# Performance work log

Measured on AMD Instinct MI355X. Metric: run time of the kernel, lower is better.

## Reference

```python
import jax, jax.numpy as jnp
import numpy as np

K = 3          # number of nearest neighbors (pointops.interpolation uses k=3)
CHUNK = 4096   # fine-point chunk size for blocked kNN (bounds peak memory)
EPS = 1e-8     # inverse-distance epsilon, matches pointops interpolation


def _interpolate(xyz1, xyz2, feature2):
    """3-NN inverse-distance weighted interpolation from coarse (xyz2, feature2)
    onto fine points xyz1. Single batch (offsets cover all points)."""
    n1 = xyz1.shape[0]
    x2_sq = jnp.sum(xyz2 * xyz2, axis=-1)  # [N2]
    chunks = xyz1.reshape(n1 // CHUNK, CHUNK, 3)

    def body(q):  # q: [CHUNK, 3]
        q_sq = jnp.sum(q * q, axis=-1, keepdims=True)          # [CHUNK, 1]
        d2 = q_sq + x2_sq[None, :] - 2.0 * (q @ xyz2.T)        # [CHUNK, N2]
        neg_d2, idx = jax.lax.top_k(-d2, K)                    # 3 smallest
        dist = jnp.sqrt(jnp.maximum(-neg_d2, 1e-12))           # euclidean
        w = 1.0 / (dist + EPS)
        w = w / jnp.sum(w, axis=-1, keepdims=True)             # [CHUNK, K]
        return jnp.einsum('qk,qkc->qc', w, feature2[idx])      # [CHUNK, C]

    out = jax.lax.map(body, chunks)  # [n_chunks, CHUNK, C]
    return out.reshape(n1, -1)


def setup_inputs() -> dict:
    key = jax.random.key(0)
    k1, k2, k3, k4, k5, k6 = jax.random.split(key, 6)
    N1, N2, C, OUT = 32768, 8192, 256, 256
    xyz1 = jax.random.normal(k1, (N1, 3), dtype=jnp.float32)
    xyz2 = jax.random.normal(k2, (N2, 3), dtype=jnp.float32)
    feature1 = jax.random.normal(k3, (N1, C), dtype=jnp.float32)
    feature2 = jax.random.normal(k4, (N2, C), dtype=jnp.float32)
    offset1 = jnp.array([N1], dtype=jnp.int32)
    offset2 = jnp.array([N2], dtype=jnp.int32)
    W = jax.random.normal(k5, (OUT, C), dtype=jnp.float32) * (1.0 / np.sqrt(C))
    b = jax.random.normal(k6, (OUT,), dtype=jnp.float32) * 0.01
    return {"xyz1": xyz1, "xyz2": xyz2, "feature1": feature1,
            "feature2": feature2, "offset1": offset1, "offset2": offset2,
            "W": W, "b": b}


def reference(xyz1, xyz2, feature1, feature2, offset1, offset2, W, b):
    interp = _interpolate(xyz1, xyz2, feature2)  # [N1, C]
    return interp @ W.T + b                      # nn.Linear(in_coarse, out)
```

## Files before the change

kernel.cpp:

```cpp
#include <hip/hip_runtime.h>


#define FLT_BIG 3.402823466e+38f
#define CAP     16
#define MARGIN  3e-5f

__device__ __forceinline__ float rlf(float v, int l) {
    return __uint_as_float((unsigned)__builtin_amdgcn_readlane((int)__float_as_uint(v), l));
}

__global__ __launch_bounds__(256) void prep_kernel(const float* __restrict__ xyz2,
                                                   float4* __restrict__ pack, int N2) {
    int j = blockIdx.x * 256 + threadIdx.x;
    if (j < N2) {
        float x = xyz2[3 * j + 0];
        float y = xyz2[3 * j + 1];
        float z = xyz2[3 * j + 2];
        float4 p;
        p.x = x; p.y = y; p.z = z;
        p.w = 0.5f * (x * x + y * y + z * z);
        pack[j] = p;
    }
}

__global__ __launch_bounds__(256) void gemm_nt_f32(const float* __restrict__ A,
                                                   const float* __restrict__ B,
                                                   float* __restrict__ C,
                                                   int M, int N, int K) {
    __shared__ float As[64][68];
    __shared__ float Bs[64][68];

    const int t  = threadIdx.x;
    const int tx = t & 15;
    const int ty = t >> 4;
    const int bm = blockIdx.x * 64;
    const int bn = blockIdx.y * 64;

    float acc[4][4] = {{0.f}};

    for (int kt = 0; kt < K; kt += 64) {
#pragma unroll
        for (int rr = 0; rr < 4; ++rr) {
            int r = ty + 16 * rr;
            int c = tx * 4;
            float4 av = *(const float4*)(A + (size_t)(bm + r) * K + kt + c);
            As[c + 0][r] = av.x;
            As[c + 1][r] = av.y;
            As[c + 2][r] = av.z;
            As[c + 3][r] = av.w;
            float4 bv = *(const float4*)(B + (size_t)(bn + r) * K + kt + c);
            Bs[c + 0][r] = bv.x;
            Bs[c + 1][r] = bv.y;
            Bs[c + 2][r] = bv.z;
            Bs[c + 3][r] = bv.w;
        }
        __syncthreads();

#pragma unroll 8
        for (int k = 0; k < 64; ++k) {
            float4 a4 = *(const float4*)&As[k][ty * 4];
            float4 b4 = *(const float4*)&Bs[k][tx * 4];
            float a[4] = {a4.x, a4.y, a4.z, a4.w};
            float b[4] = {b4.x, b4.y, b4.z, b4.w};
#pragma unroll
            for (int i = 0; i < 4; ++i)
#pragma unroll
                for (int j = 0; j < 4; ++j)
                    acc[i][j] = fmaf(a[i], b[j], acc[i][j]);
        }
        __syncthreads();
    }

#pragma unroll
    for (int i = 0; i < 4; ++i) {
        float4 v;
        v.x = acc[i][0]; v.y = acc[i][1]; v.z = acc[i][2]; v.w = acc[i][3];
        *(float4*)(C + (size_t)(bm + ty * 4 + i) * N + bn + tx * 4) = v;
    }
}

#define TOP4V_INSERT(mv)                                           \
    do {                                                           \
        float _x  = (mv);                                          \
        float _n0 = fminf(b0, _x);  float _y0 = fmaxf(b0, _x); b0 = _n0; \
        float _n1 = fminf(b1, _y0); float _y1 = fmaxf(b1, _y0); b1 = _n1; \
        float _n2 = fminf(b2, _y1); float _y2 = fmaxf(b2, _y1); b2 = _n2; \
        b3 = fminf(b3, _y2);                                       \
    } while (0)

#define TOP3JD_INSERT(dd, j)                                       \
    do {                                                           \
        bool lt2 = ((dd) < d2v) || ((dd) == d2v && (j) < j2);      \
        if (lt2) {                                                 \
            bool lt1 = ((dd) < d1) || ((dd) == d1 && (j) < j1);    \
            if (lt1) {                                             \
                d2v = d1; j2 = j1;                                 \
                bool lt0 = ((dd) < d0) || ((dd) == d0 && (j) < j0);\
                if (lt0) { d1 = d0; j1 = j0; d0 = (dd); j0 = (j); }\
                else     { d1 = (dd); j1 = (j); }                  \
            } else { d2v = (dd); j2 = (j); }                       \
        }                                                          \
    } while (0)

#define DECLS(s) float px##s, py##s, pz##s, pw##s;
#define LOADS(s) { float4 _p = pack[base + ((s) << 6) + lane]; \
                   px##s = _p.x; py##s = _p.y; pz##s = _p.z; pw##s = _p.w; }
#define SAMPW(s) samp[wave][((s) << 6) + lane] = make_float4(px##s, py##s, pz##s, pw##s);
#define SLOTF(s)                                                               \
    {                                                                          \
        float acc = fmaf(qxx, px##s, fmaf(qyy, py##s, fmaf(qzz, pz##s, tq))); \
        unsigned long long mk = __ballot(acc >= pw##s);                        \
        while (mk) {                                                           \
            int l = __builtin_ctzll(mk);                                       \
            mk &= mk - 1;                                                      \
            if (lane == 0 && cnt < CAP)                                        \
                ring[wave][q][cnt] = (unsigned short)(base + ((s) << 6) + l);  \
            ++cnt;                                                             \
        }                                                                      \
    }
#define X16(M) M(0) M(1) M(2) M(3) M(4) M(5) M(6) M(7) \
               M(8) M(9) M(10) M(11) M(12) M(13) M(14) M(15)
#define X4(M)  M(0) M(1) M(2) M(3)

__global__ __launch_bounds__(512) void knn_gather(const float* __restrict__ xyz1,
                                                  const float4* __restrict__ pack,
                                                  const float4* __restrict__ G4,
                                                  const float4* __restrict__ bias4,
                                                  float4* __restrict__ out4,
                                                  int N2) {
    __shared__ float4         samp[8][256];
    __shared__ float          md[8][64][4];
    __shared__ int            mi[8][64][3];
    __shared__ float          thr[64];
    __shared__ unsigned short ring[8][64][CAP];
    __shared__ unsigned short cnts[8][64];
    __shared__ float          swgt[64][3];
    __shared__ int            sidx[64][3];

    const int tid  = threadIdx.x;
    const int wave = __builtin_amdgcn_readfirstlane(tid >> 6);
    const int lane = tid & 63;
    const int fine = blockIdx.x * 64 + lane;

    const float qx = xyz1[3 * fine + 0];
    const float qy = xyz1[3 * fine + 1];
    const float qz = xyz1[3 * fine + 2];

    const int chunk = N2 >> 3;
    const int base  = wave * chunk;

    X16(DECLS)
    X16(LOADS)

    X4(SAMPW)
    __syncthreads();

    {
        float b0 = FLT_BIG, b1 = FLT_BIG, b2 = FLT_BIG, b3 = FLT_BIG;
        const float4* sp = samp[wave];
#pragma unroll 1
        for (int k = 0; k < 256; k += 4) {
            float4 p0 = sp[k + 0];
            float4 p1 = sp[k + 1];
            float4 p2 = sp[k + 2];
            float4 p3 = sp[k + 3];
            float m0 = p0.w - fmaf(qx, p0.x, fmaf(qy, p0.y, qz * p0.z));
            float m1 = p1.w - fmaf(qx, p1.x, fmaf(qy, p1.y, qz * p1.z));
            float m2 = p2.w - fmaf(qx, p2.x, fmaf(qy, p2.y, qz * p2.z));
            float m3 = p3.w - fmaf(qx, p3.x, fmaf(qy, p3.y, qz * p3.z));
            float mm = fminf(fminf(m0, m1), fminf(m2, m3));
            TOP4V_INSERT(mm);
        }
        md[wave][lane][0] = b0;
        md[wave][lane][1] = b1;
        md[wave][lane][2] = b2;
        md[wave][lane][3] = b3;
    }
    __syncthreads();

    if (tid < 64) {
        float b0 = FLT_BIG, b1 = FLT_BIG, b2 = FLT_BIG, b3 = FLT_BIG;
#pragma unroll
        for (int w = 0; w < 8; ++w)
#pragma unroll
            for (int k = 0; k < 4; ++k)
                TOP4V_INSERT(md[w][tid][k]);
        thr[tid] = b3 + MARGIN;
    }
    __syncthreads();

    {
        const float qt_own = thr[lane];
#pragma unroll 1
        for (int q = 0; q < 64; ++q) {
            float qxx = rlf(qx, q);
            float qyy = rlf(qy, q);
            float qzz = rlf(qz, q);
            float tq  = rlf(qt_own, q);
            int cnt = 0;
            X16(SLOTF)
            if (lane == 0) cnts[wave][q] = (unsigned short)(cnt < CAP ? cnt : CAP);
        }
    }
    __syncthreads();

    {
        const int q  = tid >> 3;
        const int w  = tid & 7;
        const int fq = blockIdx.x * 64 + q;
        const float sqx = xyz1[3 * fq + 0];
        const float sqy = xyz1[3 * fq + 1];
        const float sqz = xyz1[3 * fq + 2];
        const float qsq = __fadd_rn(__fadd_rn(__fmul_rn(sqx, sqx), __fmul_rn(sqy, sqy)),
                                    __fmul_rn(sqz, sqz));
        float d0 = FLT_BIG, d1 = FLT_BIG, d2v = FLT_BIG;
        int   j0 = 0x7fffffff, j1 = 0x7fffffff, j2 = 0x7fffffff;
        const int n = cnts[w][q];
        for (int e = 0; e < n; ++e) {
            const int j = ring[w][q][e];
            float4 p = pack[j];
            float x2s = __fadd_rn(__fadd_rn(__fmul_rn(p.x, p.x), __fmul_rn(p.y, p.y)),
                                  __fmul_rn(p.z, p.z));
            float dot = __fmaf_rn(sqz, p.z, __fmaf_rn(sqy, p.y, __fmul_rn(sqx, p.x)));
            float dd = __fsub_rn(__fadd_rn(qsq, x2s), __fmul_rn(2.0f, dot));
            TOP3JD_INSERT(dd, j);
        }
        md[w][q][0] = d0;  md[w][q][1] = d1;  md[w][q][2] = d2v;
        mi[w][q][0] = j0;  mi[w][q][1] = j1;  mi[w][q][2] = j2;
    }
    __syncthreads();

    if (tid < 64) {
        float d0 = FLT_BIG, d1 = FLT_BIG, d2v = FLT_BIG;
        int   j0 = 0x7fffffff, j1 = 0x7fffffff, j2 = 0x7fffffff;
#pragma unroll
        for (int w = 0; w < 8; ++w)
#pragma unroll
            for (int k = 0; k < 3; ++k) {
                float dd = md[w][tid][k];
                int   j  = mi[w][tid][k];
                TOP3JD_INSERT(dd, j);
            }
        float w0 = 1.0f / (__fadd_rn(sqrtf(fmaxf(d0,  1e-12f)), 1e-8f));
        float w1 = 1.0f / (__fadd_rn(sqrtf(fmaxf(d1,  1e-12f)), 1e-8f));
        float w2 = 1.0f / (__fadd_rn(sqrtf(fmaxf(d2v, 1e-12f)), 1e-8f));
        float wsum = __fadd_rn(__fadd_rn(w0, w1), w2);
        swgt[tid][0] = w0 / wsum; sidx[tid][0] = j0;
        swgt[tid][1] = w1 / wsum; sidx[tid][1] = j1;
        swgt[tid][2] = w2 / wsum; sidx[tid][2] = j2;
    }
    __syncthreads();

    const float4 bb = bias4[lane];
#pragma unroll
    for (int p = 0; p < 8; ++p) {
        int fl = wave * 8 + p;
        float w0 = swgt[fl][0];
        float w1 = swgt[fl][1];
        float w2 = swgt[fl][2];
        int j0 = sidx[fl][0];
        int j1 = sidx[fl][1];
        int j2 = sidx[fl][2];
        float4 g0 = G4[(size_t)j0 * 64 + lane];
        float4 g1 = G4[(size_t)j1 * 64 + lane];
        float4 g2 = G4[(size_t)j2 * 64 + lane];
        float4 o;
        o.x = fmaf(w0, g0.x, fmaf(w1, g1.x, fmaf(w2, g2.x, bb.x)));
        o.y = fmaf(w0, g0.y, fmaf(w1, g1.y, fmaf(w2, g2.y, bb.y)));
        o.z = fmaf(w0, g0.z, fmaf(w1, g1.z, fmaf(w2, g2.z, bb.z)));
        o.w = fmaf(w0, g0.w, fmaf(w1, g1.w, fmaf(w2, g2.w, bb.w)));
        out4[(size_t)(blockIdx.x * 64 + fl) * 64 + lane] = o;
    }
}

extern "C" void kernel_launch(void* const* d_in, const int* in_sizes, int n_in,
                              void* d_out, int out_size, void* d_ws, size_t ws_size,
                              hipStream_t stream) {
    const float* xyz1 = (const float*)d_in[0];
    const float* xyz2 = (const float*)d_in[1];
    const float* f2   = (const float*)d_in[3];
    const float* W    = (const float*)d_in[6];
    const float* bias = (const float*)d_in[7];

    const int N1  = in_sizes[0] / 3;
    const int N2  = in_sizes[1] / 3;
    const int C   = in_sizes[3] / N2;
    const int OUT = in_sizes[7];

    float*  G    = (float*)d_ws;
    float4* pack = (float4*)((char*)d_ws + (size_t)N2 * OUT * 4);

    prep_kernel<<<(N2 + 255) / 256, 256, 0, stream>>>(xyz2, pack, N2);

    dim3 ggrid(N2 / 64, OUT / 64);
    gemm_nt_f32<<<ggrid, 256, 0, stream>>>(f2, W, G, N2, OUT, C);

    knn_gather<<<N1 / 64, 512, 0, stream>>>(xyz1, pack, (const float4*)G,
                                            (const float4*)bias, (float4*)d_out, N2);
}
```

Measured before the change: 118.8 us.

## Split candidate scan into two halves to cut register pressure and raise occupancy

The threshold-filter pass now walks each wave's chunk in two halves of 8 slots, loading 32 floats per half instead of holding 64 in registers, and carries per-query counts across halves through shared memory. Launch bounds now request 4 blocks per CU, and the sample staging copies straight from global to shared. The ring and count arrays are transposed to [query][wave]. The aim is higher occupancy from fewer live registers, paid for with a second pass over the 64 queries and extra shared-memory count traffic.

```diff
diff --git a/kernel.cpp b/kernel.cpp
--- a/kernel.cpp
+++ b/kernel.cpp
@@ -103,9 +103,8 @@
     } while (0)
 
 #define DECLS(s) float px##s, py##s, pz##s, pw##s;
-#define LOADS(s) { float4 _p = pack[base + ((s) << 6) + lane]; \
+#define LOADH(s) { float4 _p = pack[jb + ((s) << 6) + lane]; \
                    px##s = _p.x; py##s = _p.y; pz##s = _p.z; pw##s = _p.w; }
-#define SAMPW(s) samp[wave][((s) << 6) + lane] = make_float4(px##s, py##s, pz##s, pw##s);
 #define SLOTF(s)                                                               \
     {                                                                          \
         float acc = fmaf(qxx, px##s, fmaf(qyy, py##s, fmaf(qzz, pz##s, tq))); \
@@ -114,26 +113,24 @@
             int l = __builtin_ctzll(mk);                                       \
             mk &= mk - 1;                                                      \
             if (lane == 0 && cnt < CAP)                                        \
-                ring[wave][q][cnt] = (unsigned short)(base + ((s) << 6) + l);  \
+                ring[q][wave][cnt] = (unsigned short)(jb + ((s) << 6) + l);    \
             ++cnt;                                                             \
         }                                                                      \
     }
-#define X16(M) M(0) M(1) M(2) M(3) M(4) M(5) M(6) M(7) \
-               M(8) M(9) M(10) M(11) M(12) M(13) M(14) M(15)
-#define X4(M)  M(0) M(1) M(2) M(3)
-
-__global__ __launch_bounds__(512) void knn_gather(const float* __restrict__ xyz1,
-                                                  const float4* __restrict__ pack,
-                                                  const float4* __restrict__ G4,
-                                                  const float4* __restrict__ bias4,
-                                                  float4* __restrict__ out4,
-                                                  int N2) {
+#define X8(M) M(0) M(1) M(2) M(3) M(4) M(5) M(6) M(7)
+
+__global__ __launch_bounds__(512, 4) void knn_gather(const float* __restrict__ xyz1,
+                                                     const float4* __restrict__ pack,
+                                                     const float4* __restrict__ G4,
+                                                     const float4* __restrict__ bias4,
+                                                     float4* __restrict__ out4,
+                                                     int N2) {
     __shared__ float4         samp[8][256];
     __shared__ float          md[8][64][4];
     __shared__ int            mi[8][64][3];
     __shared__ float          thr[64];
-    __shared__ unsigned short ring[8][64][CAP];
-    __shared__ unsigned short cnts[8][64];
+    __shared__ unsigned short ring[64][8][CAP];
+    __shared__ unsigned short cnts[64][8];
     __shared__ float          swgt[64][3];
     __shared__ int            sidx[64][3];
 
@@ -149,10 +146,9 @@
     const int chunk = N2 >> 3;
     const int base  = wave * chunk;
 
-    X16(DECLS)
-    X16(LOADS)
-
-    X4(SAMPW)
+#pragma unroll
+    for (int k = 0; k < 4; ++k)
+        samp[wave][(k << 6) + lane] = pack[base + (k << 6) + lane];
     __syncthreads();
 
     {
@@ -192,14 +188,20 @@
     {
         const float qt_own = thr[lane];
 #pragma unroll 1
-        for (int q = 0; q < 64; ++q) {
-            float qxx = rlf(qx, q);
-            float qyy = rlf(qy, q);
-            float qzz = rlf(qz, q);
-            float tq  = rlf(qt_own, q);
-            int cnt = 0;
-            X16(SLOTF)
-            if (lane == 0) cnts[wave][q] = (unsigned short)(cnt < CAP ? cnt : CAP);
+        for (int h = 0; h < 2; ++h) {
+            const int jb = base + (h << 9);
+            X8(DECLS)
+            X8(LOADH)
+#pragma unroll 1
+            for (int q = 0; q < 64; ++q) {
+                float qxx = rlf(qx, q);
+                float qyy = rlf(qy, q);
+                float qzz = rlf(qz, q);
+                float tq  = rlf(qt_own, q);
+                int cnt = h ? (int)cnts[q][wave] : 0;
+                X8(SLOTF)
+                cnts[q][wave] = (unsigned short)cnt;
+            }
         }
     }
     __syncthreads();
@@ -215,9 +217,9 @@
                                     __fmul_rn(sqz, sqz));
         float d0 = FLT_BIG, d1 = FLT_BIG, d2v = FLT_BIG;
         int   j0 = 0x7fffffff, j1 = 0x7fffffff, j2 = 0x7fffffff;
-        const int n = cnts[w][q];
+        const int n = min((int)cnts[q][w], CAP);
         for (int e = 0; e < n; ++e) {
-            const int j = ring[w][q][e];
+            const int j = ring[q][w][e];
             float4 p = pack[j];
             float x2s = __fadd_rn(__fadd_rn(__fmul_rn(p.x, p.x), __fmul_rn(p.y, p.y)),
                                   __fmul_rn(p.z, p.z));
```

Result: slower. 125.8 us (+5.9%).

## Stage full coarse point set in LDS and scan candidates per lane

Applied to the files above, without the earlier changes.

Each 512-thread block now copies all 8192 packed coarse points (128 KB) into shared memory. Candidate filtering changes from a per-query readlane/ballot loop over register-held points to a per-lane scan of the wave's 1024-point slab in LDS, with each lane writing hits to its own ring. The shared-memory scratch arrays are padded (strides of 33, 129 and 25) to avoid bank conflicts. The large LDS footprint limits occupancy to one block per CU, and N2 is now hardcoded to 8192.

```diff
diff --git a/kernel.cpp b/kernel.cpp
--- a/kernel.cpp
+++ b/kernel.cpp
@@ -4,10 +4,6 @@
 #define FLT_BIG 3.402823466e+38f
 #define CAP     16
 #define MARGIN  3e-5f
-
-__device__ __forceinline__ float rlf(float v, int l) {
-    return __uint_as_float((unsigned)__builtin_amdgcn_readlane((int)__float_as_uint(v), l));
-}
 
 __global__ __launch_bounds__(256) void prep_kernel(const float* __restrict__ xyz2,
                                                    float4* __restrict__ pack, int N2) {
@@ -102,40 +98,24 @@
         }                                                          \
     } while (0)
 
-#define DECLS(s) float px##s, py##s, pz##s, pw##s;
-#define LOADS(s) { float4 _p = pack[base + ((s) << 6) + lane]; \
-                   px##s = _p.x; py##s = _p.y; pz##s = _p.z; pw##s = _p.w; }
-#define SAMPW(s) samp[wave][((s) << 6) + lane] = make_float4(px##s, py##s, pz##s, pw##s);
-#define SLOTF(s)                                                               \
-    {                                                                          \
-        float acc = fmaf(qxx, px##s, fmaf(qyy, py##s, fmaf(qzz, pz##s, tq))); \
-        unsigned long long mk = __ballot(acc >= pw##s);                        \
-        while (mk) {                                                           \
-            int l = __builtin_ctzll(mk);                                       \
-            mk &= mk - 1;                                                      \
-            if (lane == 0 && cnt < CAP)                                        \
-                ring[wave][q][cnt] = (unsigned short)(base + ((s) << 6) + l);  \
-            ++cnt;                                                             \
-        }                                                                      \
-    }
-#define X16(M) M(0) M(1) M(2) M(3) M(4) M(5) M(6) M(7) \
-               M(8) M(9) M(10) M(11) M(12) M(13) M(14) M(15)
-#define X4(M)  M(0) M(1) M(2) M(3)
-
 __global__ __launch_bounds__(512) void knn_gather(const float* __restrict__ xyz1,
                                                   const float4* __restrict__ pack,
                                                   const float4* __restrict__ G4,
                                                   const float4* __restrict__ bias4,
                                                   float4* __restrict__ out4,
                                                   int N2) {
-    __shared__ float4         samp[8][256];
-    __shared__ float          md[8][64][4];
-    __shared__ int            mi[8][64][3];
+    __shared__ __align__(16) unsigned char slab_raw[131072];
+    __shared__ __align__(16) unsigned char ring_raw[16512];
     __shared__ float          thr[64];
-    __shared__ unsigned short ring[8][64][CAP];
-    __shared__ unsigned short cnts[8][64];
+    __shared__ unsigned short cnts[64][8];
     __shared__ float          swgt[64][3];
     __shared__ int            sidx[64][3];
+
+    float4*         slab = (float4*)slab_raw;
+    float*          mdl  = (float*)slab_raw;
+    int*            mil  = (int*)(slab_raw + 6400);
+    unsigned short* ring = (unsigned short*)ring_raw;
+    float*          mdl4 = (float*)ring_raw;
 
     const int tid  = threadIdx.x;
     const int wave = __builtin_amdgcn_readfirstlane(tid >> 6);
@@ -146,19 +126,19 @@
     const float qy = xyz1[3 * fine + 1];
     const float qz = xyz1[3 * fine + 2];
 
-    const int chunk = N2 >> 3;
-    const int base  = wave * chunk;
-
-    X16(DECLS)
-    X16(LOADS)
-
-    X4(SAMPW)
+    const int base = wave * 1024;
+
+#pragma unroll 4
+    for (int i = 0; i < 16; ++i) {
+        int idx = i * 512 + tid;
+        slab[idx] = pack[idx];
+    }
     __syncthreads();
 
     {
         float b0 = FLT_BIG, b1 = FLT_BIG, b2 = FLT_BIG, b3 = FLT_BIG;
-        const float4* sp = samp[wave];
-#pragma unroll 1
+        const float4* sp = slab + base;
+#pragma unroll 2
         for (int k = 0; k < 256; k += 4) {
             float4 p0 = sp[k + 0];
             float4 p1 = sp[k + 1];
@@ -171,10 +151,10 @@
             float mm = fminf(fminf(m0, m1), fminf(m2, m3));
             TOP4V_INSERT(mm);
         }
-        md[wave][lane][0] = b0;
-        md[wave][lane][1] = b1;
-        md[wave][lane][2] = b2;
-        md[wave][lane][3] = b3;
+        mdl4[lane * 33 + wave * 4 + 0] = b0;
+        mdl4[lane * 33 + wave * 4 + 1] = b1;
+        mdl4[lane * 33 + wave * 4 + 2] = b2;
+        mdl4[lane * 33 + wave * 4 + 3] = b3;
     }
     __syncthreads();
 
@@ -184,23 +164,38 @@
         for (int w = 0; w < 8; ++w)
 #pragma unroll
             for (int k = 0; k < 4; ++k)
-                TOP4V_INSERT(md[w][tid][k]);
+                TOP4V_INSERT(mdl4[tid * 33 + w * 4 + k]);
         thr[tid] = b3 + MARGIN;
     }
     __syncthreads();
 
     {
-        const float qt_own = thr[lane];
+        const float t = thr[lane];
+        const float4* sp = slab + base;
+        unsigned short* myring = ring + lane * 129 + wave * CAP;
+        int cnt = 0;
 #pragma unroll 1
-        for (int q = 0; q < 64; ++q) {
-            float qxx = rlf(qx, q);
-            float qyy = rlf(qy, q);
-            float qzz = rlf(qz, q);
-            float tq  = rlf(qt_own, q);
-            int cnt = 0;
-            X16(SLOTF)
-            if (lane == 0) cnts[wave][q] = (unsigned short)(cnt < CAP ? cnt : CAP);
-        }
+        for (int jj = 0; jj < 1024; jj += 4) {
+            float4 p0 = sp[jj + 0];
+            float4 p1 = sp[jj + 1];
+            float4 p2 = sp[jj + 2];
+            float4 p3 = sp[jj + 3];
+            float m0 = p0.w - fmaf(qx, p0.x, fmaf(qy, p0.y, qz * p0.z));
+            float m1 = p1.w - fmaf(qx, p1.x, fmaf(qy, p1.y, qz * p1.z));
+            float m2 = p2.w - fmaf(qx, p2.x, fmaf(qy, p2.y, qz * p2.z));
+            float m3 = p3.w - fmaf(qx, p3.x, fmaf(qy, p3.y, qz * p3.z));
+            bool a0 = m0 <= t;
+            bool a1 = m1 <= t;
+            bool a2 = m2 <= t;
+            bool a3 = m3 <= t;
+            if (__any(a0 | a1 | a2 | a3)) {
+                if (a0) { myring[min(cnt, CAP - 1)] = (unsigned short)(base + jj + 0); ++cnt; }
+                if (a1) { myring[min(cnt, CAP - 1)] = (unsigned short)(base + jj + 1); ++cnt; }
+                if (a2) { myring[min(cnt, CAP - 1)] = (unsigned short)(base + jj + 2); ++cnt; }
+                if (a3) { myring[min(cnt, CAP - 1)] = (unsigned short)(base + jj + 3); ++cnt; }
+            }
+        }
+        cnts[lane][wave] = (unsigned short)min(cnt, CAP);
     }
     __syncthreads();
 
@@ -215,9 +210,10 @@
                                     __fmul_rn(sqz, sqz));
         float d0 = FLT_BIG, d1 = FLT_BIG, d2v = FLT_BIG;
         int   j0 = 0x7fffffff, j1 = 0x7fffffff, j2 = 0x7fffffff;
-        const int n = cnts[w][q];
+        const int n = (int)cnts[q][w];
+#pragma unroll 1
         for (int e = 0; e < n; ++e) {
-            const int j = ring[w][q][e];
+            const int j = ring[q * 129 + w * CAP + e];
             float4 p = pack[j];
             float x2s = __fadd_rn(__fadd_rn(__fmul_rn(p.x, p.x), __fmul_rn(p.y, p.y)),
                                   __fmul_rn(p.z, p.z));
@@ -225,8 +221,8 @@
             float dd = __fsub_rn(__fadd_rn(qsq, x2s), __fmul_rn(2.0f, dot));
             TOP3JD_INSERT(dd, j);
         }
-        md[w][q][0] = d0;  md[w][q][1] = d1;  md[w][q][2] = d2v;
-        mi[w][q][0] = j0;  mi[w][q][1] = j1;  mi[w][q][2] = j2;
+        mdl[q * 25 + w * 3 + 0] = d0;  mdl[q * 25 + w * 3 + 1] = d1;  mdl[q * 25 + w * 3 + 2] = d2v;
+        mil[q * 25 + w * 3 + 0] = j0;  mil[q * 25 + w * 3 + 1] = j1;  mil[q * 25 + w * 3 + 2] = j2;
     }
     __syncthreads();
 
@@ -237,8 +233,8 @@
         for (int w = 0; w < 8; ++w)
 #pragma unroll
             for (int k = 0; k < 3; ++k) {
-                float dd = md[w][tid][k];
-                int   j  = mi[w][tid][k];
+                float dd = mdl[tid * 25 + w * 3 + k];
+                int   j  = mil[tid * 25 + w * 3 + k];
                 TOP3JD_INSERT(dd, j);
             }
         float w0 = 1.0f / (__fadd_rn(sqrtf(fmaxf(d0,  1e-12f)), 1e-8f));
```

New measurement: 170.6 us. 43.6% more time.
